# Performance work log

Hardware: AMD Instinct MI355X
Metric: run time of the kernel (lower is better)

## Reference

```python
import jax, jax.numpy as jnp
import numpy as np

D_MODEL = 1024
N_HEAD = 16
N_BR = 4
DH = D_MODEL // N_HEAD            # 64
H_TOT = N_BR * N_HEAD             # 64
SCALE = float(np.pi / np.sqrt(3.0))
ATTN_SCALE = DH ** -0.5


def _rope(x):
    # x: (B, H, T, Dh). Non-interleaved variant: output is cat of the two rotated halves.
    B, H, T, Dh = x.shape
    inv_freq = 1.0 / (10000.0 ** (jnp.arange(0, Dh, 2, dtype=jnp.float32) / Dh))  # (Dh/2,)
    t = jnp.arange(T, dtype=jnp.float32)
    freqs = t[:, None] * inv_freq[None, :]        # (T, Dh/2)
    cos = jnp.cos(freqs)[None, None]              # (1,1,T,Dh/2)
    sin = jnp.sin(freqs)[None, None]
    x1 = x[..., 0::2]
    x2 = x[..., 1::2]
    return jnp.concatenate([-x2 * sin + x1 * cos, x1 * sin + x2 * cos], axis=-1)


def setup_inputs() -> dict:
    key = jax.random.key(0)
    ks = jax.random.split(key, 8)
    s = 0.02
    B, T = 1, 1024
    return {
        "X": jax.random.normal(ks[0], (B, T, D_MODEL), jnp.float32),
        "Wq": jax.random.normal(ks[1], (D_MODEL, H_TOT * DH), jnp.float32) * s,
        "bq": jnp.zeros((H_TOT * DH,), jnp.float32),
        "Wk": jax.random.normal(ks[2], (D_MODEL, D_MODEL), jnp.float32) * s,
        "bk": jnp.zeros((D_MODEL,), jnp.float32),
        "Wv": jax.random.normal(ks[3], (D_MODEL, H_TOT * DH), jnp.float32) * s,
        "bv": jnp.zeros((H_TOT * DH,), jnp.float32),
        "sink_scalars": jax.random.normal(ks[4], (H_TOT, 1, 1), jnp.float32) * s,
        "v_nulls": jax.random.normal(ks[5], (H_TOT, DH), jnp.float32) * s,
        "Wo": jax.random.normal(ks[6], (D_MODEL, D_MODEL), jnp.float32) * s,
        "bo": jnp.zeros((D_MODEL,), jnp.float32),
    }


def reference(X, Wq, bq, Wk, bk, Wv, bv, sink_scalars, v_nulls, Wo, bo):
    B, T, C = X.shape
    q = (X @ Wq + bq).reshape(B, T, H_TOT, DH).transpose(0, 2, 1, 3)   # (B,H,T,Dh)
    v = (X @ Wv + bv).reshape(B, T, H_TOT, DH).transpose(0, 2, 1, 3)
    k_base = (X @ Wk + bk).reshape(B, T, N_HEAD, DH).transpose(0, 2, 1, 3)  # (B,Nh,T,Dh)
    k = jnp.tile(k_base, (1, N_BR, 1, 1))                               # (B,H,T,Dh)

    q = _rope(q)
    k = _rope(k)

    scores = jnp.einsum('bhtd,bhsd->bhts', q, k) * ATTN_SCALE           # (B,H,T,T)
    key_self = jnp.clip(jnp.sum(k * k, axis=-1), 1e-6, None)            # (B,H,T)
    denom = jnp.sqrt(key_self)[:, :, None, :]                           # (B,H,1,T)
    w = jax.nn.softplus(scores / denom)

    causal = jnp.tril(jnp.ones((T, T), dtype=bool))                     # keep lower triangle
    w = jnp.where(causal[None, None], w, 0.0)
    w = w * jax.nn.sigmoid(SCALE * w)

    sinks = jnp.tanh(sink_scalars).reshape(1, H_TOT, 1, 1) + 1e-6       # (1,H,1,1)
    alpha = 1.0 / (jnp.sum(w, axis=-1, keepdims=True) + sinks + 1e-6)   # (B,H,T,1)
    probs_tokens = w * alpha
    probs_sink = sinks * alpha                                          # (B,H,T,1)

    out_tokens = jnp.einsum('bhts,bhsd->bhtd', probs_tokens, v)
    out_sinks = probs_sink * v_nulls[None, :, None, :]                  # (B,H,T,Dh)
    context = out_tokens + out_sinks                                    # (B,H,T,Dh)

    context = context.reshape(B, N_BR, N_HEAD, T, DH)
    context = context.transpose(0, 1, 3, 2, 4).reshape(B, N_BR, T, C)
    y = context @ Wo + bo                                               # (B,N_BR,T,C)
    return jnp.mean(y, axis=1)


if __name__ == "__main__":
    out = reference(**setup_inputs())
    print(out.shape)
```

## Files before the change

### kernel.cpp

```cpp
#include <hip/hip_runtime.h>
#include <math.h>

#define SILU_SCALE 1.8137993642342178f
#define QKV_N 9216
#define LN2 0.6931471805599453f
#define DNSCALE 0.18033688011112042f

typedef __attribute__((ext_vector_type(8))) short bf16x8;
typedef __attribute__((ext_vector_type(4))) float f32x4;

#if __has_builtin(__builtin_amdgcn_exp2f)
#define EXP2(x) __builtin_amdgcn_exp2f(x)
#else
#define EXP2(x) exp2f(x)
#endif
#if __has_builtin(__builtin_amdgcn_logf)
#define LOG2(x) __builtin_amdgcn_logf(x)
#else
#define LOG2(x) __log2f(x)
#endif

__device__ __forceinline__ unsigned short f2bf(float f){
    union { float f; unsigned int i; } u; u.f = f;
    unsigned int r = u.i + 0x7FFFu + ((u.i >> 16) & 1u);
    return (unsigned short)(r >> 16);
}
__device__ __forceinline__ float bf2f(unsigned short s){
    union { unsigned int i; float f; } u; u.i = ((unsigned int)s) << 16;
    return u.f;
}
__device__ __forceinline__ unsigned int pack_bf2(float lo, float hi){
    unsigned int i0 = __float_as_uint(lo) + 0x8000u;
    unsigned int i1 = __float_as_uint(hi) + 0x8000u;
    return __builtin_amdgcn_perm(i1, i0, 0x07060302u);
}
#if __has_builtin(__builtin_amdgcn_cvt_pk_bf16_f32)
typedef __attribute__((ext_vector_type(2))) __bf16 bfp2;
__device__ __forceinline__ unsigned int pack_bf2f(float lo, float hi){
    bfp2 t = __builtin_amdgcn_cvt_pk_bf16_f32(lo, hi);
    return __builtin_bit_cast(unsigned int, t);
}
#else
__device__ __forceinline__ unsigned int pack_bf2f(float lo, float hi){
    return pack_bf2(lo, hi);
}
#endif

__device__ __forceinline__ void gload_lds16(const void* g, void* l){
    __builtin_amdgcn_global_load_lds(
        (const __attribute__((address_space(1))) void*)g,
        (__attribute__((address_space(3))) void*)l, 16, 0, 0);
}

__global__ __launch_bounds__(256) void prep_kernel(
    const float* __restrict__ X,
    const float* __restrict__ Wq, const float* __restrict__ Wk,
    const float* __restrict__ Wv, const float* __restrict__ Wo,
    const float* __restrict__ bq, const float* __restrict__ bk,
    const float* __restrict__ bv,
    unsigned short* __restrict__ Xb, unsigned short* __restrict__ WqkvT,
    unsigned short* __restrict__ WoT, float* __restrict__ qkvb)
{
    __shared__ float t[64][65];
    int b = blockIdx.x;
    const int tid = threadIdx.x;

    if (b >= 2560){
        if (b < 3072){
            int i = ((b - 2560) * 256 + tid) * 8;
            float4 a = *(const float4*)&X[i];
            float4 c = *(const float4*)&X[i + 4];
            union { unsigned short u[8]; uint4 v; } o;
            o.u[0]=f2bf(a.x); o.u[1]=f2bf(a.y); o.u[2]=f2bf(a.z); o.u[3]=f2bf(a.w);
            o.u[4]=f2bf(c.x); o.u[5]=f2bf(c.y); o.u[6]=f2bf(c.z); o.u[7]=f2bf(c.w);
            *(uint4*)&Xb[i] = o.v;
        } else {
            int i = (b - 3072) * 256 + tid;
            float v;
            if (i < 4096) v = bq[i];
            else if (i < 5120) v = bk[i - 4096];
            else v = bv[i - 5120];
            qkvb[i] = v;
        }
        return;
    }

    const float* W; unsigned short* Wt; int N, tiles_x;
    if (b < 1024)      { W = Wq; Wt = WqkvT;                       N = 4096; tiles_x = 64; }
    else if (b < 1280) { b -= 1024; W = Wk; Wt = WqkvT + (size_t)4096*1024; N = 1024; tiles_x = 16; }
    else if (b < 2304) { b -= 1280; W = Wv; Wt = WqkvT + (size_t)5120*1024; N = 4096; tiles_x = 64; }
    else               { b -= 2304; W = Wo; Wt = WoT;              N = 1024; tiles_x = 16; }

    const int k0 = (b / tiles_x) * 64, n0 = (b % tiles_x) * 64;
    const int lr  = tid >> 4;
    const int lc4 = (tid & 15) * 4;
    #pragma unroll
    for (int p = 0; p < 4; p++){
        int r = lr + p * 16;
        float4 v = *(const float4*)&W[(size_t)(k0 + r) * N + n0 + lc4];
        t[lc4+0][r] = v.x; t[lc4+1][r] = v.y;
        t[lc4+2][r] = v.z; t[lc4+3][r] = v.w;
    }
    __syncthreads();
    const int wr  = tid >> 3;
    const int wc8 = (tid & 7) * 8;
    #pragma unroll
    for (int p = 0; p < 2; p++){
        int r = wr + p * 32;
        union { unsigned short u[8]; uint4 v; } o;
        #pragma unroll
        for (int j = 0; j < 8; j++) o.u[j] = f2bf(t[r][wc8 + j]);
        *(uint4*)&Wt[(size_t)(n0 + r) * 1024 + k0 + wc8] = o.v;
    }
}

template<int BM, int BN, int OUTBF>
__global__ __launch_bounds__(256) void gemm_k(
    const unsigned short* __restrict__ A,
    const unsigned short* __restrict__ Bt,
    const float* __restrict__ bias,
    void* __restrict__ Cout, int M, int N, int K)
{
    constexpr int MT = BM / 32;
    constexpr int NT = BN / 32;
    __shared__ unsigned short As[BM * 64];
    __shared__ unsigned short Bs[BN * 64];
    const int tid  = threadIdx.x;
    const int wave = tid >> 6;
    const int lane = tid & 63;
    const int l15  = lane & 15;
    const int quad = lane >> 4;
    const int m0 = blockIdx.y * BM;
    const int n0 = blockIdx.x * BN;
    const int wm = (wave >> 1) * (BM / 2);
    const int wn = (wave & 1) * (BN / 2);

    f32x4 acc[MT][NT];
    #pragma unroll
    for (int i = 0; i < MT; i++)
        #pragma unroll
        for (int j = 0; j < NT; j++)
            acc[i][j] = (f32x4){0.f, 0.f, 0.f, 0.f};

    for (int k0 = 0; k0 < K; k0 += 64){
        #pragma unroll
        for (int j = 0; j < (BM * 8) / 256; j++){
            int bslot = j * 256 + wave * 64;
            int slot = bslot + lane;
            int row = slot >> 3, phys = slot & 7;
            int c = phys ^ (row & 7);
            gload_lds16(&A[(size_t)(m0 + row) * K + k0 + c * 8], &As[bslot * 8]);
        }
        #pragma unroll
        for (int j = 0; j < (BN * 8) / 256; j++){
            int bslot = j * 256 + wave * 64;
            int slot = bslot + lane;
            int row = slot >> 3, phys = slot & 7;
            int c = phys ^ (row & 7);
            gload_lds16(&Bt[(size_t)(n0 + row) * K + k0 + c * 8], &Bs[bslot * 8]);
        }
        __syncthreads();
        #pragma unroll
        for (int ks = 0; ks < 2; ks++){
            bf16x8 af[MT], bfr[NT];
            #pragma unroll
            for (int i = 0; i < MT; i++){
                int row = wm + i * 16 + l15;
                int phys = (ks * 4 + quad) ^ (row & 7);
                af[i] = *(const bf16x8*)&As[row * 64 + phys * 8];
            }
            #pragma unroll
            for (int j = 0; j < NT; j++){
                int row = wn + j * 16 + l15;
                int phys = (ks * 4 + quad) ^ (row & 7);
                bfr[j] = *(const bf16x8*)&Bs[row * 64 + phys * 8];
            }
            #pragma unroll
            for (int i = 0; i < MT; i++)
                #pragma unroll
                for (int j = 0; j < NT; j++)
                    acc[i][j] = __builtin_amdgcn_mfma_f32_16x16x32_bf16(af[i], bfr[j], acc[i][j], 0, 0, 0);
        }
        __syncthreads();
    }
    #pragma unroll
    for (int i = 0; i < MT; i++){
        #pragma unroll
        for (int j = 0; j < NT; j++){
            int col = n0 + wn + j * 16 + l15;
            float bv = bias[col];
            #pragma unroll
            for (int r = 0; r < 4; r++){
                int row = m0 + wm + i * 16 + quad * 4 + r;
                float v = acc[i][j][r] + bv;
                if (OUTBF) ((unsigned short*)Cout)[(size_t)row * N + col] = f2bf(v);
                else       ((float*)Cout)[(size_t)row * N + col] = v;
            }
        }
    }
}

__global__ __launch_bounds__(256) void gemm_wo(
    const unsigned short* __restrict__ A,
    const unsigned short* __restrict__ Bt,
    float* __restrict__ P)
{
    constexpr int BM = 128, BN = 64, MT = 4, NT = 2;
    __shared__ unsigned short As[BM * 64];
    __shared__ unsigned short Bs[BN * 64];
    const int tid  = threadIdx.x;
    const int wave = tid >> 6;
    const int lane = tid & 63;
    const int l15  = lane & 15;
    const int quad = lane >> 4;
    const int m0 = blockIdx.y * BM;
    const int n0 = blockIdx.x * BN;
    const int kz = blockIdx.z;
    const int wm = (wave >> 1) * 64;
    const int wn = (wave & 1) * 32;

    f32x4 acc[MT][NT];
    #pragma unroll
    for (int i = 0; i < MT; i++)
        #pragma unroll
        for (int j = 0; j < NT; j++)
            acc[i][j] = (f32x4){0.f, 0.f, 0.f, 0.f};

    const int kbeg = kz * 512;
    for (int k0 = kbeg; k0 < kbeg + 512; k0 += 64){
        #pragma unroll
        for (int j = 0; j < (BM * 8) / 256; j++){
            int bslot = j * 256 + wave * 64;
            int slot = bslot + lane;
            int row = slot >> 3, phys = slot & 7;
            int c = phys ^ (row & 7);
            gload_lds16(&A[(size_t)(m0 + row) * 1024 + k0 + c * 8], &As[bslot * 8]);
        }
        #pragma unroll
        for (int j = 0; j < (BN * 8) / 256; j++){
            int bslot = j * 256 + wave * 64;
            int slot = bslot + lane;
            int row = slot >> 3, phys = slot & 7;
            int c = phys ^ (row & 7);
            gload_lds16(&Bt[(size_t)(n0 + row) * 1024 + k0 + c * 8], &Bs[bslot * 8]);
        }
        __syncthreads();
        #pragma unroll
        for (int ks = 0; ks < 2; ks++){
            bf16x8 af[MT], bfr[NT];
            #pragma unroll
            for (int i = 0; i < MT; i++){
                int row = wm + i * 16 + l15;
                int phys = (ks * 4 + quad) ^ (row & 7);
                af[i] = *(const bf16x8*)&As[row * 64 + phys * 8];
            }
            #pragma unroll
            for (int j = 0; j < NT; j++){
                int row = wn + j * 16 + l15;
                int phys = (ks * 4 + quad) ^ (row & 7);
                bfr[j] = *(const bf16x8*)&Bs[row * 64 + phys * 8];
            }
            #pragma unroll
            for (int i = 0; i < MT; i++)
                #pragma unroll
                for (int j = 0; j < NT; j++)
                    acc[i][j] = __builtin_amdgcn_mfma_f32_16x16x32_bf16(af[i], bfr[j], acc[i][j], 0, 0, 0);
        }
        __syncthreads();
    }
    float* Pz = P + (size_t)kz * 1024 * 1024;
    #pragma unroll
    for (int i = 0; i < MT; i++){
        #pragma unroll
        for (int j = 0; j < NT; j++){
            int col = n0 + wn + j * 16 + l15;
            #pragma unroll
            for (int r = 0; r < 4; r++){
                int row = m0 + wm + i * 16 + quad * 4 + r;
                Pz[(size_t)row * 1024 + col] = acc[i][j][r];
            }
        }
    }
}

__global__ void wo_reduce(const float* __restrict__ P, const float* __restrict__ bo,
                          float* __restrict__ out)
{
    int i = (blockIdx.x * 256 + threadIdx.x) * 4;
    float4 a = *(const float4*)&P[i];
    float4 b = *(const float4*)&P[1024 * 1024 + i];
    float4 c = *(const float4*)&bo[i & 1023];
    float4 o;
    o.x = a.x + b.x + c.x; o.y = a.y + b.y + c.y;
    o.z = a.z + b.z + c.z; o.w = a.w + b.w + c.w;
    *(float4*)&out[i] = o;
}

__global__ __launch_bounds__(256) void postproc_kernel(
    unsigned short* __restrict__ qkv, unsigned short* __restrict__ VT)
{
    int b = blockIdx.x;
    const int tid = threadIdx.x;
    if (b < 64){
        int idx = b * 256 + tid;
        int t = idx >> 4, h = idx & 15;
        unsigned short* p = qkv + (size_t)t * QKV_N + 4096 + h * 64;
        uint4 raw[8];
        #pragma unroll
        for (int i = 0; i < 8; i++) raw[i] = *(const uint4*)(p + i * 8);
        const unsigned short* rp = (const unsigned short*)raw;
        float x[64];
        #pragma unroll
        for (int i = 0; i < 64; i++) x[i] = bf2f(rp[i]);
        float ra[32], rb[32];
        float ss = 0.f;
        #pragma unroll
        for (int d = 0; d < 32; d++){
            float inv = EXP2(-(float)d * 0.4152410118609203f);
            float s, c; __sincosf((float)t * inv, &s, &c);
            float x1 = x[2*d], x2 = x[2*d+1];
            float a = x1 * c - x2 * s;
            float bb = x1 * s + x2 * c;
            ss = fmaf(a, a, fmaf(bb, bb, ss));
            ra[d] = a; rb[d] = bb;
        }
        float scale = DNSCALE * rsqrtf(fmaxf(ss, 1e-6f));
        unsigned short o[64];
        #pragma unroll
        for (int d = 0; d < 32; d++){
            o[d]      = f2bf(ra[d] * scale);
            o[d + 32] = f2bf(rb[d] * scale);
        }
        #pragma unroll
        for (int i = 0; i < 8; i++) *(uint4*)(p + i * 8) = ((const uint4*)o)[i];
        return;
    }
    b -= 64;
    const int h = b >> 4, s0 = (b & 15) * 64;
    __shared__ unsigned short tile[64 * 64];
    const unsigned short* V = qkv + 5120;
    const int pr = tid >> 3, cch = tid & 7;
    uint4 g0 = *(const uint4*)&V[(size_t)(s0 + 2 * pr)     * QKV_N + h * 64 + cch * 8];
    uint4 g1 = *(const uint4*)&V[(size_t)(s0 + 2 * pr + 1) * QKV_N + h * 64 + cch * 8];
    const unsigned short* p0 = (const unsigned short*)&g0;
    const unsigned short* p1 = (const unsigned short*)&g1;
    #pragma unroll
    for (int j = 0; j < 8; j++){
        int d = cch * 8 + j;
        int physc = (pr >> 2) ^ ((d ^ (d >> 3)) & 7);
        unsigned int val = (unsigned int)p0[j] | ((unsigned int)p1[j] << 16);
        ((unsigned int*)tile)[d * 32 + physc * 4 + (pr & 3)] = val;
    }
    __syncthreads();
    #pragma unroll
    for (int i = 0; i < 2; i++){
        int slot = tid + i * 256;
        int d = slot >> 3, c = slot & 7;
        int phys = c ^ ((d ^ (d >> 3)) & 7);
        uint4 v = *(const uint4*)&tile[d * 64 + phys * 8];
        *(uint4*)&VT[((size_t)h * 64 + d) * 1024 + s0 + c * 8] = v;
    }
}

__global__ __launch_bounds__(256) void attn_mfma(
    const unsigned short* __restrict__ qkv,
    const unsigned short* __restrict__ VT,
    const float* __restrict__ sinks, const float* __restrict__ vnulls,
    unsigned short* __restrict__ ctx)
{
    __shared__ unsigned short ks[64 * 64];
    __shared__ unsigned short vt[64 * 64];
    __shared__ unsigned short ws[64][72];

    const int tid  = threadIdx.x;
    const int wave = tid >> 6;
    const int lane = tid & 63;
    const int l15  = lane & 15;
    const int quad = lane >> 4;
    const int h  = blockIdx.x;
    const int kh = h & 15;
    const int qt = 15 - blockIdx.y;
    const int t0 = qt << 6;

    const unsigned short* Q  = qkv;
    const unsigned short* Kp = qkv + 4096;
    const unsigned short* Vh = VT + (size_t)h * 64 * 1024;

    const int srow0 = tid >> 3,         sphy0 = tid & 7;
    const int srow1 = (tid + 256) >> 3, sphy1 = tid & 7;
    const int sc0 = sphy0 ^ (srow0 & 7);
    const int sc1 = sphy1 ^ (srow1 & 7);

    bf16x8 qf0, qf1;
    {
        const int t = t0 + wave * 16 + l15;
        const unsigned short* qp = Q + (size_t)t * QKV_N + h * 64 + quad * 16;
        uint4 r0 = *(const uint4*)qp;
        uint4 r1 = *(const uint4*)(qp + 8);
        unsigned short e[16];
        *(uint4*)&e[0] = r0; *(uint4*)&e[8] = r1;
        unsigned short o0[8], o1[8];
        #pragma unroll
        for (int j = 0; j < 8; j++){
            int dp = quad * 8 + j;
            float inv = EXP2(-(float)dp * 0.4152410118609203f);
            float s, c; __sincosf((float)t * inv, &s, &c);
            float x1 = bf2f(e[2*j]), x2 = bf2f(e[2*j+1]);
            o0[j] = f2bf(x1 * c - x2 * s);
            o1[j] = f2bf(x1 * s + x2 * c);
        }
        qf0 = *(const bf16x8*)o0;
        qf1 = *(const bf16x8*)o1;
    }

    bf16x8 ones;
    {
        union { unsigned short u[8]; bf16x8 v; } o;
        #pragma unroll
        for (int j = 0; j < 8; j++) o.u[j] = 0x3F80;
        ones = o.v;
    }

    f32x4 acc_o[4];
    #pragma unroll
    for (int i = 0; i < 4; i++) acc_o[i] = (f32x4){0.f, 0.f, 0.f, 0.f};
    f32x4 acc_den = (f32x4){0.f, 0.f, 0.f, 0.f};
    const int q_glob = t0 + wave * 16 + l15;

    uint4 kr0, kr1, vr0, vr1;
    {
        kr0 = *(const uint4*)&Kp[(size_t)srow0 * QKV_N + kh * 64 + sc0 * 8];
        kr1 = *(const uint4*)&Kp[(size_t)srow1 * QKV_N + kh * 64 + sc1 * 8];
        vr0 = *(const uint4*)&Vh[(size_t)srow0 * 1024 + sc0 * 8];
        vr1 = *(const uint4*)&Vh[(size_t)srow1 * 1024 + sc1 * 8];
    }

    for (int st = 0; st <= qt; st++){
        const int s0 = st << 6;
        __syncthreads();

        *(uint4*)&ks[(size_t)tid * 8]         = kr0;
        *(uint4*)&ks[(size_t)(tid + 256) * 8] = kr1;
        *(uint4*)&vt[(size_t)tid * 8]         = vr0;
        *(uint4*)&vt[(size_t)(tid + 256) * 8] = vr1;

        if (st < qt){
            const int sn = (st + 1) << 6;
            kr0 = *(const uint4*)&Kp[(size_t)(sn + srow0) * QKV_N + kh * 64 + sc0 * 8];
            kr1 = *(const uint4*)&Kp[(size_t)(sn + srow1) * QKV_N + kh * 64 + sc1 * 8];
            vr0 = *(const uint4*)&Vh[(size_t)srow0 * 1024 + sn + sc0 * 8];
            vr1 = *(const uint4*)&Vh[(size_t)srow1 * 1024 + sn + sc1 * 8];
        }
        __syncthreads();

        const bool diag = (st == qt);

        #pragma unroll
        for (int nt = 0; nt < 4; nt++){
            const int sbase = nt * 16 + quad * 4;
            uint2* wp = (uint2*)&ws[wave * 16 + l15][sbase];
            if (diag && nt > wave){ *wp = (uint2){0u, 0u}; continue; }

            f32x4 sc = (f32x4){0.f, 0.f, 0.f, 0.f};
            {
                int srow = nt * 16 + l15;
                int ph0 = quad ^ (srow & 7);
                int ph1 = (4 + quad) ^ (srow & 7);
                bf16x8 kf0 = *(const bf16x8*)&ks[srow * 64 + ph0 * 8];
                bf16x8 kf1 = *(const bf16x8*)&ks[srow * 64 + ph1 * 8];
                sc = __builtin_amdgcn_mfma_f32_16x16x32_bf16(kf0, qf0, sc, 0, 0, 0);
                sc = __builtin_amdgcn_mfma_f32_16x16x32_bf16(kf1, qf1, sc, 0, 0, 0);
            }
            float w4[4];
            if (!diag){
                #pragma unroll
                for (int r = 0; r < 4; r++){
                    float y = sc[r];
                    float p = EXP2(-fabsf(y));
                    float u = fmaxf(y, 0.f) + LOG2(1.f + p);
                    float e3 = EXP2(-SILU_SCALE * u);
                    w4[r] = __fdividef(u, 1.f + e3);
                }
            } else {
                #pragma unroll
                for (int r = 0; r < 4; r++){
                    float y = sc[r];
                    float p = EXP2(-fabsf(y));
                    float u = fmaxf(y, 0.f) + LOG2(1.f + p);
                    float e3 = EXP2(-SILU_SCALE * u);
                    float wv = __fdividef(u, 1.f + e3);
                    w4[r] = (s0 + sbase + r <= q_glob) ? wv : 0.f;
                }
            }
            uint2 pk;
            pk.x = pack_bf2f(w4[0], w4[1]);
            pk.y = pack_bf2f(w4[2], w4[3]);
            *wp = pk;
        }

        {
            const int prow = wave * 16 + l15;
            bf16x8 pf0 = *(const bf16x8*)&ws[prow][quad * 8];
            bf16x8 pf1 = *(const bf16x8*)&ws[prow][32 + quad * 8];
            const bool skip_hi = diag && (wave <= 1);
            #pragma unroll
            for (int dt = 0; dt < 4; dt++){
                int d = dt * 16 + l15;
                int sw = d & 7;
                bf16x8 vf0 = *(const bf16x8*)&vt[d * 64 + (quad ^ sw) * 8];
                acc_o[dt] = __builtin_amdgcn_mfma_f32_16x16x32_bf16(pf0, vf0, acc_o[dt], 0, 0, 0);
                if (!skip_hi){
                    bf16x8 vf1 = *(const bf16x8*)&vt[d * 64 + ((4 + quad) ^ sw) * 8];
                    acc_o[dt] = __builtin_amdgcn_mfma_f32_16x16x32_bf16(pf1, vf1, acc_o[dt], 0, 0, 0);
                }
            }
            acc_den = __builtin_amdgcn_mfma_f32_16x16x32_bf16(pf0, ones, acc_den, 0, 0, 0);
            if (!skip_hi)
                acc_den = __builtin_amdgcn_mfma_f32_16x16x32_bf16(pf1, ones, acc_den, 0, 0, 0);
        }
    }

    float sinkv = tanhf(sinks[h]) + 1e-6f;
    #pragma unroll
    for (int r = 0; r < 4; r++){
        int qg = t0 + wave * 16 + quad * 4 + r;
        float alpha = __fdividef(1.f, LN2 * acc_den[r] + sinkv + 1e-6f);
        #pragma unroll
        for (int dt = 0; dt < 4; dt++){
            int d = dt * 16 + l15;
            float o = (LN2 * acc_o[dt][r] + sinkv * vnulls[h * 64 + d]) * alpha;
            ctx[((size_t)h * 1024 + qg) * 64 + d] = f2bf(o);
        }
    }
}

__global__ void avg_kernel(const unsigned short* __restrict__ ctx, unsigned short* __restrict__ avg)
{
    int i8 = (blockIdx.x * 256 + threadIdx.x) * 8;
    int t = i8 >> 10, c = i8 & 1023;
    int nh = c >> 6, d = c & 63;
    float s[8] = {};
    #pragma unroll
    for (int br = 0; br < 4; br++){
        uint4 v = *(const uint4*)&ctx[((size_t)(br * 16 + nh) * 1024 + t) * 64 + d];
        const unsigned short* p = (const unsigned short*)&v;
        #pragma unroll
        for (int j = 0; j < 8; j++) s[j] += bf2f(p[j]);
    }
    union { unsigned short u[8]; uint4 v; } o;
    #pragma unroll
    for (int j = 0; j < 8; j++) o.u[j] = f2bf(0.25f * s[j]);
    *(uint4*)&avg[i8] = o.v;
}

extern "C" void kernel_launch(void* const* d_in, const int* in_sizes, int n_in,
                              void* d_out, int out_size, void* d_ws, size_t ws_size,
                              hipStream_t stream)
{
    (void)in_sizes; (void)n_in; (void)out_size; (void)ws_size;
    const float* X      = (const float*)d_in[0];
    const float* Wq     = (const float*)d_in[1];
    const float* bq     = (const float*)d_in[2];
    const float* Wk     = (const float*)d_in[3];
    const float* bk     = (const float*)d_in[4];
    const float* Wv     = (const float*)d_in[5];
    const float* bv     = (const float*)d_in[6];
    const float* sinks  = (const float*)d_in[7];
    const float* vnulls = (const float*)d_in[8];
    const float* Wo     = (const float*)d_in[9];
    const float* bo     = (const float*)d_in[10];
    float* out = (float*)d_out;

    unsigned short* w16   = (unsigned short*)d_ws;
    unsigned short* Xb    = w16;
    unsigned short* WqkvT = Xb    + (size_t)1024 * 1024;
    unsigned short* QKVb  = WqkvT + (size_t)QKV_N * 1024;
    unsigned short* WoT   = QKVb  + (size_t)1024 * QKV_N;
    unsigned short* ctxb  = WoT   + (size_t)1024 * 1024;
    unsigned short* avgb  = ctxb  + (size_t)64 * 1024 * 64;
    float* qkvb = (float*)(avgb + (size_t)1024 * 1024);
    unsigned short* VTb = WqkvT;
    float* pWo = (float*)(WqkvT + (size_t)4 * 1024 * 1024);

    dim3 blk(256);
    prep_kernel<<<3108, blk, 0, stream>>>(X, Wq, Wk, Wv, Wo, bq, bk, bv,
                                          Xb, WqkvT, WoT, qkvb);
    gemm_k<128, 96, 1><<<dim3(96, 8), blk, 0, stream>>>(Xb, WqkvT, qkvb, QKVb, 1024, QKV_N, 1024);
    postproc_kernel<<<1088, blk, 0, stream>>>(QKVb, VTb);
    attn_mfma<<<dim3(64, 16), blk, 0, stream>>>(QKVb, VTb, sinks, vnulls, ctxb);
    avg_kernel<<<512, blk, 0, stream>>>(ctxb, avgb);
    gemm_wo<<<dim3(16, 8, 2), blk, 0, stream>>>(avgb, WoT, pWo);
    wo_reduce<<<1024, blk, 0, stream>>>(pWo, bo, out);
}
```

Before: 185.2 us.

## Register-prefetch next K tile in GEMMs instead of direct global-to-LDS loads

Both GEMM kernels drop the direct global_load_lds path. They now load the next K tile into registers while the current tile is computed, then store it to LDS at the start of the next iteration. The aim is to hide global load latency behind the MFMA work within a single LDS buffer. The cost is extra VGPRs for the staging registers, an explicit LDS write per tile, and a barrier layout that moves the sync to before the compute.

```diff
diff --git a/kernel.cpp b/kernel.cpp
--- a/kernel.cpp
+++ b/kernel.cpp
@@ -45,12 +45,6 @@
     return pack_bf2(lo, hi);
 }
 #endif
-
-__device__ __forceinline__ void gload_lds16(const void* g, void* l){
-    __builtin_amdgcn_global_load_lds(
-        (const __attribute__((address_space(1))) void*)g,
-        (__attribute__((address_space(3))) void*)l, 16, 0, 0);
-}
 
 __global__ __launch_bounds__(256) void prep_kernel(
     const float* __restrict__ X,
@@ -123,6 +117,8 @@
 {
     constexpr int MT = BM / 32;
     constexpr int NT = BN / 32;
+    constexpr int ASL = (BM * 8) / 256;
+    constexpr int BSL = (BN * 8) / 256;
     __shared__ unsigned short As[BM * 64];
     __shared__ unsigned short Bs[BN * 64];
     const int tid  = threadIdx.x;
@@ -135,6 +131,20 @@
     const int wm = (wave >> 1) * (BM / 2);
     const int wn = (wave & 1) * (BN / 2);
 
+    int arow[ASL], acol[ASL], brow[BSL], bcol[BSL];
+    #pragma unroll
+    for (int i = 0; i < ASL; i++){
+        int slot = i * 256 + tid;
+        arow[i] = slot >> 3;
+        acol[i] = (slot & 7) ^ (arow[i] & 7);
+    }
+    #pragma unroll
+    for (int i = 0; i < BSL; i++){
+        int slot = i * 256 + tid;
+        brow[i] = slot >> 3;
+        bcol[i] = (slot & 7) ^ (brow[i] & 7);
+    }
+
     f32x4 acc[MT][NT];
     #pragma unroll
     for (int i = 0; i < MT; i++)
@@ -142,24 +152,33 @@
         for (int j = 0; j < NT; j++)
             acc[i][j] = (f32x4){0.f, 0.f, 0.f, 0.f};
 
+    uint4 ar[ASL], br[BSL];
+    #pragma unroll
+    for (int i = 0; i < ASL; i++)
+        ar[i] = *(const uint4*)&A[(size_t)(m0 + arow[i]) * K + acol[i] * 8];
+    #pragma unroll
+    for (int i = 0; i < BSL; i++)
+        br[i] = *(const uint4*)&Bt[(size_t)(n0 + brow[i]) * K + bcol[i] * 8];
+
     for (int k0 = 0; k0 < K; k0 += 64){
-        #pragma unroll
-        for (int j = 0; j < (BM * 8) / 256; j++){
-            int bslot = j * 256 + wave * 64;
-            int slot = bslot + lane;
-            int row = slot >> 3, phys = slot & 7;
-            int c = phys ^ (row & 7);
-            gload_lds16(&A[(size_t)(m0 + row) * K + k0 + c * 8], &As[bslot * 8]);
-        }
-        #pragma unroll
-        for (int j = 0; j < (BN * 8) / 256; j++){
-            int bslot = j * 256 + wave * 64;
-            int slot = bslot + lane;
-            int row = slot >> 3, phys = slot & 7;
-            int c = phys ^ (row & 7);
-            gload_lds16(&Bt[(size_t)(n0 + row) * K + k0 + c * 8], &Bs[bslot * 8]);
-        }
         __syncthreads();
+        #pragma unroll
+        for (int i = 0; i < ASL; i++)
+            *(uint4*)&As[(size_t)(i * 256 + tid) * 8] = ar[i];
+        #pragma unroll
+        for (int i = 0; i < BSL; i++)
+            *(uint4*)&Bs[(size_t)(i * 256 + tid) * 8] = br[i];
+
+        if (k0 + 64 < K){
+            #pragma unroll
+            for (int i = 0; i < ASL; i++)
+                ar[i] = *(const uint4*)&A[(size_t)(m0 + arow[i]) * K + k0 + 64 + acol[i] * 8];
+            #pragma unroll
+            for (int i = 0; i < BSL; i++)
+                br[i] = *(const uint4*)&Bt[(size_t)(n0 + brow[i]) * K + k0 + 64 + bcol[i] * 8];
+        }
+        __syncthreads();
+
         #pragma unroll
         for (int ks = 0; ks < 2; ks++){
             bf16x8 af[MT], bfr[NT];
@@ -181,7 +200,6 @@
                 for (int j = 0; j < NT; j++)
                     acc[i][j] = __builtin_amdgcn_mfma_f32_16x16x32_bf16(af[i], bfr[j], acc[i][j], 0, 0, 0);
         }
-        __syncthreads();
     }
     #pragma unroll
     for (int i = 0; i < MT; i++){
@@ -206,6 +224,7 @@
     float* __restrict__ P)
 {
     constexpr int BM = 128, BN = 64, MT = 4, NT = 2;
+    constexpr int ASL = 4, BSL = 2;
     __shared__ unsigned short As[BM * 64];
     __shared__ unsigned short Bs[BN * 64];
     const int tid  = threadIdx.x;
@@ -219,6 +238,20 @@
     const int wm = (wave >> 1) * 64;
     const int wn = (wave & 1) * 32;
 
+    int arow[ASL], acol[ASL], brow[BSL], bcol[BSL];
+    #pragma unroll
+    for (int i = 0; i < ASL; i++){
+        int slot = i * 256 + tid;
+        arow[i] = slot >> 3;
+        acol[i] = (slot & 7) ^ (arow[i] & 7);
+    }
+    #pragma unroll
+    for (int i = 0; i < BSL; i++){
+        int slot = i * 256 + tid;
+        brow[i] = slot >> 3;
+        bcol[i] = (slot & 7) ^ (brow[i] & 7);
+    }
+
     f32x4 acc[MT][NT];
     #pragma unroll
     for (int i = 0; i < MT; i++)
@@ -227,24 +260,33 @@
             acc[i][j] = (f32x4){0.f, 0.f, 0.f, 0.f};
 
     const int kbeg = kz * 512;
+    uint4 ar[ASL], br[BSL];
+    #pragma unroll
+    for (int i = 0; i < ASL; i++)
+        ar[i] = *(const uint4*)&A[(size_t)(m0 + arow[i]) * 1024 + kbeg + acol[i] * 8];
+    #pragma unroll
+    for (int i = 0; i < BSL; i++)
+        br[i] = *(const uint4*)&Bt[(size_t)(n0 + brow[i]) * 1024 + kbeg + bcol[i] * 8];
+
     for (int k0 = kbeg; k0 < kbeg + 512; k0 += 64){
-        #pragma unroll
-        for (int j = 0; j < (BM * 8) / 256; j++){
-            int bslot = j * 256 + wave * 64;
-            int slot = bslot + lane;
-            int row = slot >> 3, phys = slot & 7;
-            int c = phys ^ (row & 7);
-            gload_lds16(&A[(size_t)(m0 + row) * 1024 + k0 + c * 8], &As[bslot * 8]);
-        }
-        #pragma unroll
-        for (int j = 0; j < (BN * 8) / 256; j++){
-            int bslot = j * 256 + wave * 64;
-            int slot = bslot + lane;
-            int row = slot >> 3, phys = slot & 7;
-            int c = phys ^ (row & 7);
-            gload_lds16(&Bt[(size_t)(n0 + row) * 1024 + k0 + c * 8], &Bs[bslot * 8]);
-        }
         __syncthreads();
+        #pragma unroll
+        for (int i = 0; i < ASL; i++)
+            *(uint4*)&As[(size_t)(i * 256 + tid) * 8] = ar[i];
+        #pragma unroll
+        for (int i = 0; i < BSL; i++)
+            *(uint4*)&Bs[(size_t)(i * 256 + tid) * 8] = br[i];
+
+        if (k0 + 64 < kbeg + 512){
+            #pragma unroll
+            for (int i = 0; i < ASL; i++)
+                ar[i] = *(const uint4*)&A[(size_t)(m0 + arow[i]) * 1024 + k0 + 64 + acol[i] * 8];
+            #pragma unroll
+            for (int i = 0; i < BSL; i++)
+                br[i] = *(const uint4*)&Bt[(size_t)(n0 + brow[i]) * 1024 + k0 + 64 + bcol[i] * 8];
+        }
+        __syncthreads();
+
         #pragma unroll
         for (int ks = 0; ks < 2; ks++){
             bf16x8 af[MT], bfr[NT];
@@ -266,7 +308,6 @@
                 for (int j = 0; j < NT; j++)
                     acc[i][j] = __builtin_amdgcn_mfma_f32_16x16x32_bf16(af[i], bfr[j], acc[i][j], 0, 0, 0);
         }
-        __syncthreads();
     }
     float* Pz = P + (size_t)kz * 1024 * 1024;
     #pragma unroll
```

Result: slower. 264.5 us (+42.8%).
